# Performance work log

Hardware: AMD Instinct MI355X
Metric: run time of the kernel (lower is better)

Reference implementation:

```python
import jax, jax.numpy as jnp
import numpy as np

EPS = 1e-5

def setup_inputs() -> dict:
    key = jax.random.key(0)
    k0, k1 = jax.random.split(key, 2)
    N6, M5, M4 = 524288, 131072, 32768
    Cin, Cout = 256, 512
    data = jax.random.normal(k0, (N6, Cin), dtype=jnp.float32)
    weight = jax.random.normal(k1, (Cout, Cin), dtype=jnp.float32) * (1.0 / np.sqrt(Cin))
    gamma = jnp.ones((Cout,), dtype=jnp.float32)
    beta = jnp.zeros((Cout,), dtype=jnp.float32)
    # indices of non-empty nodes at the coarser depth (sorted, unique):
    # depth 6 has N6/8 = 65536 parents among M5 = 131072 depth-5 nodes (stride 2)
    idx5 = (jnp.arange(N6 // 8, dtype=jnp.int32) * (M5 // (N6 // 8)))
    # depth 5 has M5/8 = 16384 parents among M4 = 32768 depth-4 nodes (stride 2)
    idx4 = (jnp.arange(M5 // 8, dtype=jnp.int32) * (M4 // (M5 // 8)))
    return {"data": data, "weight": weight, "gamma": gamma, "beta": beta,
            "idx5": idx5, "idx4": idx4, "nnum5": M5, "nnum4": M4,
            "in_depth": 6, "out_depth": 4}

def _octree_max_pool(x, idx, nnum):
    # x: [N, C] child features in sibling groups of 8 -> pooled [N/8, C],
    # scattered (octree_pad) into the full coarser level of size nnum.
    N, C = x.shape
    y = x.reshape(N // 8, 8, C).max(axis=1)
    return jnp.zeros((nnum, C), x.dtype).at[idx].set(y)

def reference(data, weight, gamma, beta, idx5, idx4, nnum5, nnum4, in_depth, out_depth):
    out = data
    # in_depth (6) > out_depth (4): pool twice, then conv1x1+BN+ReLU
    for idx, nnum in ((idx5, nnum5), (idx4, nnum4)):
        out = _octree_max_pool(out, idx, nnum)
    h = out @ weight.T                      # 1x1 conv == bias-free linear
    mean = h.mean(axis=0)
    var = h.var(axis=0)
    h = (h - mean) * jax.lax.rsqrt(var + EPS) * gamma + beta
    return jax.nn.relu(h)
```

## Files before the change

kernel.cpp:

```cpp
#include <hip/hip_runtime.h>
#include <hip/hip_bf16.h>
#include <math.h>

#define CIN 256
#define COUT 512

typedef __attribute__((ext_vector_type(8))) short bf16x8;
typedef __attribute__((ext_vector_type(4))) float f32x4;
typedef __attribute__((ext_vector_type(4))) float f32x4v;

__device__ __forceinline__ ushort f2bf(float f) {
    union { float f; unsigned u; } x; x.f = f;
    unsigned r = x.u + 0x7FFFu + ((x.u >> 16) & 1u);
    return (ushort)(r >> 16);
}
__device__ __forceinline__ float bf2f(ushort u) {
    union { unsigned u; float f; } x; x.u = (unsigned)u << 16; return x.f;
}

__global__ __launch_bounds__(256) void prep_kernel(const int* __restrict__ idx5, int n_i5,
                                                   const int* __restrict__ idx4, int n_i4,
                                                   int n5, int n4,
                                                   int* __restrict__ inv5, int* __restrict__ inv4,
                                                   const float* __restrict__ W,
                                                   ushort* __restrict__ Wb, int wquads) {
    int t = blockIdx.x * blockDim.x + threadIdx.x;
    if (t < n_i5) {
        int s = idx5[t];
        inv5[s] = t;
        int e = (t + 1 < n_i5) ? idx5[t + 1] : n5;
        for (int k = s + 1; k < e; ++k) inv5[k] = -1;
        if (t == 0) for (int k = 0; k < s; ++k) inv5[k] = -1;
    } else if (t < n_i5 + n_i4) {
        int i = t - n_i5;
        int s = idx4[i];
        inv4[s] = i;
        int e = (i + 1 < n_i4) ? idx4[i + 1] : n4;
        for (int k = s + 1; k < e; ++k) inv4[k] = -1;
        if (i == 0) for (int k = 0; k < s; ++k) inv4[k] = -1;
    } else if (t < n_i5 + n_i4 + wquads) {
        int i = (t - n_i5 - n_i4) * 4;
        float4 v = *reinterpret_cast<const float4*>(W + i);
        ushort4 o;
        o.x = f2bf(v.x); o.y = f2bf(v.y); o.z = f2bf(v.z); o.w = f2bf(v.w);
        *reinterpret_cast<ushort4*>(&Wb[i]) = o;
    }
}

__global__ __launch_bounds__(256) void pool2_kernel(const float* __restrict__ data,
                                                    const int* __restrict__ inv5,
                                                    ushort* __restrict__ P, int G2) {
    int t = blockIdx.x * blockDim.x + threadIdx.x;
    int g = t >> 6;
    int q = t & 63;
    if (g >= G2) return;

    float4 acc = make_float4(-INFINITY, -INFINITY, -INFINITY, -INFINITY);
    bool any_empty = false;

    #pragma unroll
    for (int s = 0; s < 8; ++s) {
        int i = inv5[g * 8 + s];
        i = __builtin_amdgcn_readfirstlane(i);
        if (i >= 0) {
            const float* base = data + (size_t)i * 8 * CIN + q * 4;
            #pragma unroll
            for (int r = 0; r < 8; ++r) {
                f32x4v v = __builtin_nontemporal_load(
                    reinterpret_cast<const f32x4v*>(base + (size_t)r * CIN));
                acc.x = fmaxf(acc.x, v.x);
                acc.y = fmaxf(acc.y, v.y);
                acc.z = fmaxf(acc.z, v.z);
                acc.w = fmaxf(acc.w, v.w);
            }
        } else {
            any_empty = true;
        }
    }
    if (any_empty) {
        acc.x = fmaxf(acc.x, 0.f);
        acc.y = fmaxf(acc.y, 0.f);
        acc.z = fmaxf(acc.z, 0.f);
        acc.w = fmaxf(acc.w, 0.f);
    }
    ushort4 o;
    o.x = f2bf(acc.x); o.y = f2bf(acc.y); o.z = f2bf(acc.z); o.w = f2bf(acc.w);
    *reinterpret_cast<ushort4*>(&P[(size_t)g * CIN + q * 4]) = o;
}

__global__ __launch_bounds__(256) void mfma_gemm_kernel(const ushort* __restrict__ A,
                                                        const ushort* __restrict__ B,
                                                        ushort* __restrict__ H,
                                                        float* __restrict__ partial) {
    __shared__ __align__(16) ushort Asm[128 * 64];
    __shared__ __align__(16) ushort Bsm[128 * 64];

    int t = threadIdx.x;
    int lane = t & 63;
    int wid = t >> 6;
    int wm = wid >> 1, wn = wid & 1;
    int m0 = blockIdx.x * 128, n0 = blockIdx.y * 128;

    f32x4 acc[4][4] = {};

    for (int k0 = 0; k0 < CIN; k0 += 64) {
        #pragma unroll
        for (int i = 0; i < 4; ++i) {
            int idx = i * 256 + t;
            int row = idx >> 3;
            int sl  = idx & 7;
            bf16x8 av = *reinterpret_cast<const bf16x8*>(A + (size_t)(m0 + row) * CIN + k0 + sl * 8);
            bf16x8 bv = *reinterpret_cast<const bf16x8*>(B + (size_t)(n0 + row) * CIN + k0 + sl * 8);
            int ws = (sl ^ (row & 7)) * 8;
            *reinterpret_cast<bf16x8*>(&Asm[row * 64 + ws]) = av;
            *reinterpret_cast<bf16x8*>(&Bsm[row * 64 + ws]) = bv;
        }
        __syncthreads();

        #pragma unroll
        for (int ks = 0; ks < 2; ++ks) {
            bf16x8 af[4], bfr[4];
            int slog = ks * 4 + (lane >> 4);
            #pragma unroll
            for (int mi = 0; mi < 4; ++mi) {
                int row = wm * 64 + mi * 16 + (lane & 15);
                af[mi] = *reinterpret_cast<const bf16x8*>(&Asm[row * 64 + (slog ^ (row & 7)) * 8]);
            }
            #pragma unroll
            for (int ni = 0; ni < 4; ++ni) {
                int col = wn * 64 + ni * 16 + (lane & 15);
                bfr[ni] = *reinterpret_cast<const bf16x8*>(&Bsm[col * 64 + (slog ^ (col & 7)) * 8]);
            }
            #pragma unroll
            for (int mi = 0; mi < 4; ++mi)
                #pragma unroll
                for (int ni = 0; ni < 4; ++ni)
                    acc[mi][ni] = __builtin_amdgcn_mfma_f32_16x16x32_bf16(af[mi], bfr[ni], acc[mi][ni], 0, 0, 0);
        }
        __syncthreads();
    }

    float s[4], q[4];
    #pragma unroll
    for (int ni = 0; ni < 4; ++ni) {
        s[ni] = 0.f; q[ni] = 0.f;
        #pragma unroll
        for (int mi = 0; mi < 4; ++mi)
            #pragma unroll
            for (int r = 0; r < 4; ++r) {
                float v = acc[mi][ni][r];
                s[ni] += v;
                q[ni] = fmaf(v, v, q[ni]);
            }
        s[ni] += __shfl_xor(s[ni], 16);
        s[ni] += __shfl_xor(s[ni], 32);
        q[ni] += __shfl_xor(q[ni], 16);
        q[ni] += __shfl_xor(q[ni], 32);
    }
    float* redS = (float*)Asm;
    float* redQ = redS + 256;
    if (lane < 16) {
        #pragma unroll
        for (int ni = 0; ni < 4; ++ni) {
            int c = wn * 64 + ni * 16 + lane;
            redS[wm * 128 + c] = s[ni];
            redQ[wm * 128 + c] = q[ni];
        }
    }
    __syncthreads();
    if (t < 128) {
        float S = redS[t] + redS[128 + t];
        float Q = redQ[t] + redQ[128 + t];
        partial[(size_t)blockIdx.x * 1024 + blockIdx.y * 128 + t]       = S;
        partial[(size_t)blockIdx.x * 1024 + 512 + blockIdx.y * 128 + t] = Q;
    }

    #pragma unroll
    for (int mi = 0; mi < 4; ++mi) {
        #pragma unroll
        for (int ni = 0; ni < 4; ++ni) {
            int col   = n0 + wn * 64 + ni * 16 + (lane & 15);
            int rbase = m0 + wm * 64 + mi * 16 + (lane >> 4) * 4;
            #pragma unroll
            for (int r = 0; r < 4; ++r)
                H[(size_t)(rbase + r) * COUT + col] = f2bf(acc[mi][ni][r]);
        }
    }
}

__global__ __launch_bounds__(256) void bn_finalize_kernel(const float* __restrict__ partial, int nparts,
                                                          const float* __restrict__ gamma,
                                                          const float* __restrict__ beta,
                                                          float* __restrict__ scale,
                                                          float* __restrict__ shift,
                                                          float invN) {
    int c = blockIdx.x * blockDim.x + threadIdx.x;
    if (c >= COUT) return;
    float s = 0.f, q = 0.f;
    for (int p = 0; p < nparts; ++p) {
        s += partial[(size_t)p * 1024 + c];
        q += partial[(size_t)p * 1024 + 512 + c];
    }
    float mean = s * invN;
    float var  = fmaf(q, invN, -mean * mean);
    float inv  = rsqrtf(var + 1e-5f);
    float sc   = gamma[c] * inv;
    scale[c] = sc;
    shift[c] = fmaf(-mean, sc, beta[c]);
}

__global__ __launch_bounds__(256) void out_kernel(const ushort* __restrict__ H,
                                                  const int* __restrict__ inv4,
                                                  const float* __restrict__ scale,
                                                  const float* __restrict__ shift,
                                                  float* __restrict__ out, int rows) {
    int t = blockIdx.x * blockDim.x + threadIdx.x;
    int m = t >> 7;
    int qd = t & 127;
    if (m >= rows) return;
    int c = qd * 4;
    int j = inv4[m];
    float4 sc = *reinterpret_cast<const float4*>(&scale[c]);
    float4 sh = *reinterpret_cast<const float4*>(&shift[c]);
    float4 r;
    if (j >= 0) {
        ushort4 h = *reinterpret_cast<const ushort4*>(&H[(size_t)j * COUT + c]);
        r.x = fmaxf(fmaf(bf2f(h.x), sc.x, sh.x), 0.f);
        r.y = fmaxf(fmaf(bf2f(h.y), sc.y, sh.y), 0.f);
        r.z = fmaxf(fmaf(bf2f(h.z), sc.z, sh.z), 0.f);
        r.w = fmaxf(fmaf(bf2f(h.w), sc.w, sh.w), 0.f);
    } else {
        r.x = fmaxf(sh.x, 0.f);
        r.y = fmaxf(sh.y, 0.f);
        r.z = fmaxf(sh.z, 0.f);
        r.w = fmaxf(sh.w, 0.f);
    }
    *reinterpret_cast<float4*>(&out[(size_t)m * COUT + c]) = r;
}

extern "C" void kernel_launch(void* const* d_in, const int* in_sizes, int n_in,
                              void* d_out, int out_size, void* d_ws, size_t ws_size,
                              hipStream_t stream) {
    const float* data   = (const float*)d_in[0];
    const float* weight = (const float*)d_in[1];
    const float* gamma  = (const float*)d_in[2];
    const float* beta   = (const float*)d_in[3];
    const int*   idx5   = (const int*)d_in[4];
    const int*   idx4   = (const int*)d_in[5];

    const int n_i5 = in_sizes[4];
    const int n_i4 = in_sizes[5];
    const int G2   = n_i4;
    const int n5   = 8 * n_i4;
    const int rows = out_size / COUT;
    const int M    = G2;
    const int MB   = M / 128;

    char* w = (char*)d_ws;
    ushort* P      = (ushort*)w;                        w += (size_t)G2 * CIN * sizeof(ushort);
    ushort* H      = (ushort*)w;                        w += (size_t)G2 * COUT * sizeof(ushort);
    ushort* Wb     = (ushort*)w;                        w += (size_t)COUT * CIN * sizeof(ushort);
    float* partial = (float*)w;                         w += (size_t)MB * 1024 * sizeof(float);
    float* scale   = (float*)w;                         w += COUT * sizeof(float);
    float* shift   = (float*)w;                         w += COUT * sizeof(float);
    int*   inv5    = (int*)w;                           w += (size_t)n5 * sizeof(int);
    int*   inv4    = (int*)w;                           w += (size_t)rows * sizeof(int);

    const int wquads = COUT * CIN / 4;

    {
        int n = n_i5 + n_i4 + wquads;
        prep_kernel<<<(n + 255) / 256, 256, 0, stream>>>(idx5, n_i5, idx4, n_i4, n5, rows,
                                                         inv5, inv4, weight, Wb, wquads);
    }
    pool2_kernel<<<(G2 * 64 + 255) / 256, 256, 0, stream>>>(data, inv5, P, G2);
    {
        dim3 grid(MB, COUT / 128);
        mfma_gemm_kernel<<<grid, 256, 0, stream>>>(P, Wb, H, partial);
    }
    bn_finalize_kernel<<<2, 256, 0, stream>>>(partial, MB, gamma, beta, scale, shift,
                                              1.0f / (float)rows);
    out_kernel<<<((size_t)rows * 128 + 255) / 256, 256, 0, stream>>>(H, inv4, scale, shift,
                                                                     (float*)d_out, rows);
}
```

Measured before the change: 155.9 us.

## Fuse prep and pooling kernels, replace inv5 table with per-block binary search

Merges the index-inversion/weight-conversion prep kernel with the two-level max-pool kernel into one launch, with extra blocks handling weight bf16 conversion and inv4 construction. The inv5 inverse map is no longer materialized; each pool block binary-searches idx5 for its 32 depth-5 slots into shared memory. This removes one kernel launch and the dependent global write/read of inv5, at the cost of log-depth searches per block and a block-level barrier before the streaming loads.

```diff
diff --git a/kernel.cpp b/kernel.cpp
--- a/kernel.cpp
+++ b/kernel.cpp
@@ -18,52 +18,68 @@
     union { unsigned u; float f; } x; x.u = (unsigned)u << 16; return x.f;
 }
 
-__global__ __launch_bounds__(256) void prep_kernel(const int* __restrict__ idx5, int n_i5,
-                                                   const int* __restrict__ idx4, int n_i4,
-                                                   int n5, int n4,
-                                                   int* __restrict__ inv5, int* __restrict__ inv4,
-                                                   const float* __restrict__ W,
-                                                   ushort* __restrict__ Wb, int wquads) {
-    int t = blockIdx.x * blockDim.x + threadIdx.x;
-    if (t < n_i5) {
-        int s = idx5[t];
-        inv5[s] = t;
-        int e = (t + 1 < n_i5) ? idx5[t + 1] : n5;
-        for (int k = s + 1; k < e; ++k) inv5[k] = -1;
-        if (t == 0) for (int k = 0; k < s; ++k) inv5[k] = -1;
-    } else if (t < n_i5 + n_i4) {
-        int i = t - n_i5;
-        int s = idx4[i];
-        inv4[s] = i;
-        int e = (i + 1 < n_i4) ? idx4[i + 1] : n4;
-        for (int k = s + 1; k < e; ++k) inv4[k] = -1;
-        if (i == 0) for (int k = 0; k < s; ++k) inv4[k] = -1;
-    } else if (t < n_i5 + n_i4 + wquads) {
-        int i = (t - n_i5 - n_i4) * 4;
-        float4 v = *reinterpret_cast<const float4*>(W + i);
-        ushort4 o;
-        o.x = f2bf(v.x); o.y = f2bf(v.y); o.z = f2bf(v.z); o.w = f2bf(v.w);
-        *reinterpret_cast<ushort4*>(&Wb[i]) = o;
-    }
-}
-
-__global__ __launch_bounds__(256) void pool2_kernel(const float* __restrict__ data,
-                                                    const int* __restrict__ inv5,
-                                                    ushort* __restrict__ P, int G2) {
-    int t = blockIdx.x * blockDim.x + threadIdx.x;
-    int g = t >> 6;
-    int q = t & 63;
-    if (g >= G2) return;
+__device__ __forceinline__ int bsearch_eq(const int* __restrict__ arr, int n, int key) {
+    int lo = 0, hi = n - 1;
+    while (lo <= hi) {
+        int mid = (lo + hi) >> 1;
+        int v = arr[mid];
+        if (v == key) return mid;
+        if (v < key) lo = mid + 1; else hi = mid - 1;
+    }
+    return -1;
+}
+
+__global__ __launch_bounds__(256) void pool_prep_kernel(const float* __restrict__ data,
+                                                        const int* __restrict__ idx5, int n_i5,
+                                                        const int* __restrict__ idx4, int n_i4,
+                                                        const float* __restrict__ W,
+                                                        ushort* __restrict__ Wb,
+                                                        ushort* __restrict__ P, int G2,
+                                                        int* __restrict__ inv4, int n4) {
+    const int b = blockIdx.x;
+    const int nPool = G2 >> 2;
+    const int t = threadIdx.x;
+
+    if (b >= nPool) {
+        int rb = b - nPool;
+        if (rb < 32) {
+            int q0 = rb * 1024 + t;
+            #pragma unroll
+            for (int j = 0; j < 4; ++j) {
+                int i = (q0 + j * 256) * 4;
+                float4 v = *reinterpret_cast<const float4*>(W + i);
+                ushort4 o;
+                o.x = f2bf(v.x); o.y = f2bf(v.y); o.z = f2bf(v.z); o.w = f2bf(v.w);
+                *reinterpret_cast<ushort4*>(&Wb[i]) = o;
+            }
+        } else {
+            int i = (rb - 32) * 256 + t;
+            if (i < n_i4) {
+                int s = idx4[i];
+                inv4[s] = i;
+                int e = (i + 1 < n_i4) ? idx4[i + 1] : n4;
+                for (int k = s + 1; k < e; ++k) inv4[k] = -1;
+                if (i == 0) for (int k = 0; k < s; ++k) inv4[k] = -1;
+            }
+        }
+        return;
+    }
+
+    __shared__ int inv5_l[32];
+    if (t < 32) inv5_l[t] = bsearch_eq(idx5, n_i5, b * 32 + t);
+    __syncthreads();
+
+    const int w = t >> 6, lane = t & 63;
+    const int g = b * 4 + w;
 
     float4 acc = make_float4(-INFINITY, -INFINITY, -INFINITY, -INFINITY);
     bool any_empty = false;
-
     #pragma unroll
     for (int s = 0; s < 8; ++s) {
-        int i = inv5[g * 8 + s];
+        int i = inv5_l[w * 8 + s];
         i = __builtin_amdgcn_readfirstlane(i);
         if (i >= 0) {
-            const float* base = data + (size_t)i * 8 * CIN + q * 4;
+            const float* base = data + (size_t)i * (8 * CIN) + lane * 4;
             #pragma unroll
             for (int r = 0; r < 8; ++r) {
                 f32x4v v = __builtin_nontemporal_load(
@@ -85,7 +101,7 @@
     }
     ushort4 o;
     o.x = f2bf(acc.x); o.y = f2bf(acc.y); o.z = f2bf(acc.z); o.w = f2bf(acc.w);
-    *reinterpret_cast<ushort4*>(&P[(size_t)g * CIN + q * 4]) = o;
+    *reinterpret_cast<ushort4*>(&P[(size_t)g * CIN + lane * 4]) = o;
 }
 
 __global__ __launch_bounds__(256) void mfma_gemm_kernel(const ushort* __restrict__ A,
@@ -152,10 +168,8 @@
                 s[ni] += v;
                 q[ni] = fmaf(v, v, q[ni]);
             }
-        s[ni] += __shfl_xor(s[ni], 16);
-        s[ni] += __shfl_xor(s[ni], 32);
-        q[ni] += __shfl_xor(q[ni], 16);
-        q[ni] += __shfl_xor(q[ni], 32);
+        s[ni] += __shfl_xor(s[ni], 16); s[ni] += __shfl_xor(s[ni], 32);
+        q[ni] += __shfl_xor(q[ni], 16); q[ni] += __shfl_xor(q[ni], 32);
     }
     float* redS = (float*)Asm;
     float* redQ = redS + 256;
@@ -251,7 +265,6 @@
     const int n_i5 = in_sizes[4];
     const int n_i4 = in_sizes[5];
     const int G2   = n_i4;
-    const int n5   = 8 * n_i4;
     const int rows = out_size / COUT;
     const int M    = G2;
     const int MB   = M / 128;
@@ -263,17 +276,11 @@
     float* partial = (float*)w;                         w += (size_t)MB * 1024 * sizeof(float);
     float* scale   = (float*)w;                         w += COUT * sizeof(float);
     float* shift   = (float*)w;                         w += COUT * sizeof(float);
-    int*   inv5    = (int*)w;                           w += (size_t)n5 * sizeof(int);
     int*   inv4    = (int*)w;                           w += (size_t)rows * sizeof(int);
 
-    const int wquads = COUT * CIN / 4;
-
-    {
-        int n = n_i5 + n_i4 + wquads;
-        prep_kernel<<<(n + 255) / 256, 256, 0, stream>>>(idx5, n_i5, idx4, n_i4, n5, rows,
-                                                         inv5, inv4, weight, Wb, wquads);
-    }
-    pool2_kernel<<<(G2 * 64 + 255) / 256, 256, 0, stream>>>(data, inv5, P, G2);
+    pool_prep_kernel<<<G2 / 4 + 32 + (n_i4 + 255) / 256, 256, 0, stream>>>(
+        data, idx5, n_i5, idx4, n_i4, weight, Wb, P, G2, inv4, rows);
+
     {
         dim3 grid(MB, COUT / 128);
         mfma_gemm_kernel<<<grid, 256, 0, stream>>>(P, Wb, H, partial);
```

New measurement: 155.1 us. Within noise of the previous version (-0.5%).
